# Performance work log

Hardware: AMD Instinct MI355X
Metric: run time of the kernel (lower is better)

Reference implementation:

```python
import jax, jax.numpy as jnp
import numpy as np

NUM_ITERATIONS = 3

def squash(t, axis=-1):
    sq = jnp.sum(t * t, axis=axis, keepdims=True)
    scale = sq / (1.0 + sq)
    return scale * t / jnp.sqrt(sq)

def setup_inputs() -> dict:
    key = jax.random.key(0)
    k1, k2 = jax.random.split(key)
    B, N, Ci = 16, 1024, 64
    C, O = 32, 32
    x = jax.random.normal(k1, (B, N, Ci), dtype=jnp.float32)
    route_weights = jax.random.normal(k2, (C, N, Ci, O), dtype=jnp.float32)
    return {"x": x, "route_weights": route_weights}

def reference(x, route_weights):
    # priors: (C, B, N, O)  == torch's (C,B,N,1,O) with singleton squeezed
    priors = jnp.einsum('bni,cnio->cbno', x, route_weights)
    C, B, N, O = priors.shape
    logits = jnp.zeros((C, B, N, 1), dtype=priors.dtype)
    outputs = None
    for i in range(NUM_ITERATIONS):
        probs = jax.nn.softmax(logits, axis=2)  # over route nodes
        outputs = squash(jnp.sum(probs * priors, axis=2, keepdims=True))  # (C,B,1,O)
        if i != NUM_ITERATIONS - 1:
            delta = jnp.sum(priors * outputs, axis=-1, keepdims=True)  # (C,B,N,1)
            logits = logits + delta
    # match torch output shape (C, B, 1, 1, O)
    return outputs[:, :, :, None, :]
```

## Files before the change

kernel.cpp:

```cpp
#include <hip/hip_runtime.h>

constexpr int kB  = 16;
constexpr int kN  = 1024;
constexpr int kCI = 64;
constexpr int kC  = 32;
constexpr int kO  = 32;
constexpr int kNT = 4;

#define AS1(p) ((__attribute__((address_space(1))) void*)(p))
#define AS3(p) ((__attribute__((address_space(3))) void*)(p))

__global__ __launch_bounds__(128) void priors_kernel(
    const float* __restrict__ x,
    const float* rw,
    float* priors, int cstride, int bstride, int nstr) {
  const int c  = blockIdx.x >> 8;
  const int n0 = (blockIdx.x & 255) * kNT;
  const int t  = threadIdx.x;

  __shared__ float ws[kNT * kCI * kO];

  {
    const float4* src = (const float4*)(rw + (size_t)(c * kN + n0) * (kCI * kO));
    float4* dst4 = (float4*)ws;
    #pragma unroll
    for (int it = 0; it < 16; ++it) {
      int f = t + 128 * it;
      __builtin_amdgcn_global_load_lds(AS1(const_cast<float4*>(src + f)),
                                       AS3(dst4 + f), 16, 0, 0);
    }
  }
  __syncthreads();

  const int j  = t >> 5;
  const int og = (t & 31) >> 2;
  const int bg = t & 3;
  const float* wp  = ws + j * (kCI * kO) + og * 4;
  const float* xr0 = x + (size_t)(bg * 4) * (kN * kCI) + (size_t)(n0 + j) * kCI;

  float acc[4][4];
  #pragma unroll
  for (int bb = 0; bb < 4; ++bb)
    #pragma unroll
    for (int oo = 0; oo < 4; ++oo) acc[bb][oo] = 0.f;

  #pragma unroll
  for (int i0 = 0; i0 < kCI; i0 += 4) {
    float4 wv[4], xv[4];
    #pragma unroll
    for (int q = 0; q < 4; ++q) wv[q] = *(const float4*)(wp + (i0 + q) * kO);
    #pragma unroll
    for (int bb = 0; bb < 4; ++bb)
      xv[bb] = *(const float4*)(xr0 + (size_t)bb * (kN * kCI) + i0);
    #pragma unroll
    for (int q = 0; q < 4; ++q) {
      const float* wq = (const float*)&wv[q];
      #pragma unroll
      for (int bb = 0; bb < 4; ++bb) {
        const float xq = ((const float*)&xv[bb])[q];
        #pragma unroll
        for (int oo = 0; oo < 4; ++oo)
          acc[bb][oo] += xq * wq[oo];
      }
    }
  }

  float* dst = priors + (size_t)c * cstride + (size_t)(n0 + j) * nstr + og * 4;
  #pragma unroll
  for (int bb = 0; bb < 4; ++bb) {
    int b = bg * 4 + bb;
    float4 v = make_float4(acc[bb][0], acc[bb][1], acc[bb][2], acc[bb][3]);
    *(float4*)(dst + (size_t)b * bstride) = v;
  }
}

__global__ __launch_bounds__(256) void routing_kernel(
    const float* priors, int cstride, int bstride, int nstr,
    float* __restrict__ out) {
  const int cb = blockIdx.x;
  const int c = cb >> 4, b = cb & 15;
  const int t = threadIdx.x;

  __shared__ float R[256 * 33];
  __shared__ float S2[8 * 33];
  __shared__ float out_lds[kO];
  __shared__ float wred[8];

  const float* base = priors + (size_t)c * cstride + (size_t)b * bstride;

  float p[4][kO];
  #pragma unroll
  for (int k = 0; k < 4; ++k) {
    const float* rp = base + (size_t)(t + 256 * k) * nstr;
    #pragma unroll
    for (int q = 0; q < 8; ++q) {
      float4 v = *(const float4*)(rp + q * 4);
      p[k][q * 4 + 0] = v.x; p[k][q * 4 + 1] = v.y;
      p[k][q * 4 + 2] = v.z; p[k][q * 4 + 3] = v.w;
    }
  }

  float l[4] = {0.f, 0.f, 0.f, 0.f};

  for (int iter = 0; iter < 3; ++iter) {
    if (iter > 0) {
      #pragma unroll
      for (int k = 0; k < 4; ++k) {
        float d = 0.f;
        #pragma unroll
        for (int o = 0; o < kO; ++o) d += p[k][o] * out_lds[o];
        l[k] += d;
      }
    }
    float lm = fmaxf(fmaxf(l[0], l[1]), fmaxf(l[2], l[3]));
    #pragma unroll
    for (int s = 32; s >= 1; s >>= 1) lm = fmaxf(lm, __shfl_xor(lm, s));
    if ((t & 63) == 0) wred[t >> 6] = lm;
    __syncthreads();
    const float m = fmaxf(fmaxf(wred[0], wred[1]), fmaxf(wred[2], wred[3]));

    float acc[kO];
    #pragma unroll
    for (int o = 0; o < kO; ++o) acc[o] = 0.f;
    float denp = 0.f;
    #pragma unroll
    for (int k = 0; k < 4; ++k) {
      float e = __expf(l[k] - m);
      denp += e;
      #pragma unroll
      for (int o = 0; o < kO; ++o) acc[o] += e * p[k][o];
    }
    #pragma unroll
    for (int s = 32; s >= 1; s >>= 1) denp += __shfl_xor(denp, s);
    if ((t & 63) == 0) wred[4 + (t >> 6)] = denp;

    #pragma unroll
    for (int o = 0; o < kO; ++o) R[t * 33 + o] = acc[o];
    __syncthreads();
    {
      int o = t & 31, g = t >> 5;
      float s = 0.f;
      #pragma unroll
      for (int jj = 0; jj < 32; ++jj) s += R[(g * 32 + jj) * 33 + o];
      S2[g * 33 + o] = s;
    }
    __syncthreads();
    if (t < kO) {
      float s = 0.f;
      #pragma unroll
      for (int g = 0; g < 8; ++g) s += S2[g * 33 + t];
      const float den = wred[4] + wred[5] + wred[6] + wred[7];
      s /= den;
      float sq = s * s;
      #pragma unroll
      for (int sh = 16; sh >= 1; sh >>= 1) sq += __shfl_xor(sq, sh);
      const float r = sqrtf(sq);
      const float ov = s * (r / (1.f + sq));
      out_lds[t] = ov;
      if (iter == 2) out[cb * kO + t] = ov;
    }
    __syncthreads();
  }
}

extern "C" void kernel_launch(void* const* d_in, const int* in_sizes, int n_in,
                              void* d_out, int out_size, void* d_ws, size_t ws_size,
                              hipStream_t stream) {
  const float* x  = (const float*)d_in[0];
  const float* rw = (const float*)d_in[1];
  float* out = (float*)d_out;

  const size_t need = (size_t)kC * kN * kB * kO * sizeof(float);
  float* priors;
  int cstride, bstride, nstr;
  if (ws_size >= need) {
    priors  = (float*)d_ws;
    cstride = kB * kN * kO;
    bstride = kN * kO;
    nstr    = kO;
  } else {
    priors  = (float*)const_cast<float*>(rw);
    cstride = kN * kCI * kO;
    bstride = kO;
    nstr    = kCI * kO;
  }

  priors_kernel<<<dim3(kC * (kN / kNT)), dim3(128), 0, stream>>>(
      x, rw, priors, cstride, bstride, nstr);
  routing_kernel<<<dim3(kC * kB), dim3(256), 0, stream>>>(
      priors, cstride, bstride, nstr, out);
}
```

Baseline: 434.7 us.

## Process multiple capsules per priors block with LDS-resident x and double-buffered weights

The priors kernel now has each block handle eight capsules for the same group of four route nodes. The x slice is loaded once into LDS in a transposed, batch-contiguous layout and reused across all eight capsules, replacing repeated global reads of x. Route weights for the next capsule are staged into a second LDS buffer while the current one is computed, aiming to hide load latency. In exchange the grid shrinks eightfold and LDS use per block grows to about 80 KB, which lowers occupancy and may limit how much latency can be hidden.

```diff
diff --git a/kernel.cpp b/kernel.cpp
--- a/kernel.cpp
+++ b/kernel.cpp
@@ -6,6 +6,7 @@
 constexpr int kC  = 32;
 constexpr int kO  = 32;
 constexpr int kNT = 4;
+constexpr int kCL = 8;
 
 #define AS1(p) ((__attribute__((address_space(1))) void*)(p))
 #define AS3(p) ((__attribute__((address_space(3))) void*)(p))
@@ -14,20 +15,41 @@
     const float* __restrict__ x,
     const float* rw,
     float* priors, int cstride, int bstride, int nstr) {
-  const int c  = blockIdx.x >> 8;
-  const int n0 = (blockIdx.x & 255) * kNT;
+  const int ng = blockIdx.x & 255;
+  const int c0 = (blockIdx.x >> 8) * kCL;
+  const int n0 = ng * kNT;
   const int t  = threadIdx.x;
 
-  __shared__ float ws[kNT * kCI * kO];
+  __shared__ float ws[2][kNT * kCI * kO];
+  __shared__ float xs[kNT * kCI * kB];
+
+#define STAGE_RW(buf, cc) do {                                               \
+    const float4* _src =                                                     \
+        (const float4*)(rw + (size_t)((cc) * kN + n0) * (kCI * kO));         \
+    float4* _dst = (float4*)ws[buf];                                         \
+    _Pragma("unroll")                                                        \
+    for (int _it = 0; _it < 16; ++_it) {                                     \
+      int _f = t + 128 * _it;                                                \
+      __builtin_amdgcn_global_load_lds(AS1(const_cast<float4*>(_src + _f)),  \
+                                       AS3(_dst + _f), 16, 0, 0);            \
+    }                                                                        \
+  } while (0)
+
+  STAGE_RW(0, c0);
 
   {
-    const float4* src = (const float4*)(rw + (size_t)(c * kN + n0) * (kCI * kO));
-    float4* dst4 = (float4*)ws;
-    #pragma unroll
-    for (int it = 0; it < 16; ++it) {
+    #pragma unroll
+    for (int it = 0; it < 8; ++it) {
       int f = t + 128 * it;
-      __builtin_amdgcn_global_load_lds(AS1(const_cast<float4*>(src + f)),
-                                       AS3(dst4 + f), 16, 0, 0);
+      int b = f & 15;
+      int a = (f >> 4) & 15;
+      int j = f >> 8;
+      float4 v = *(const float4*)(x + (size_t)(b * kN + n0 + j) * kCI + a * 4);
+      int idx = (j * kCI + a * 4) * kB + b;
+      xs[idx +  0] = v.x;
+      xs[idx + 16] = v.y;
+      xs[idx + 32] = v.z;
+      xs[idx + 48] = v.w;
     }
   }
   __syncthreads();
@@ -35,43 +57,51 @@
   const int j  = t >> 5;
   const int og = (t & 31) >> 2;
   const int bg = t & 3;
-  const float* wp  = ws + j * (kCI * kO) + og * 4;
-  const float* xr0 = x + (size_t)(bg * 4) * (kN * kCI) + (size_t)(n0 + j) * kCI;
-
-  float acc[4][4];
-  #pragma unroll
-  for (int bb = 0; bb < 4; ++bb)
-    #pragma unroll
-    for (int oo = 0; oo < 4; ++oo) acc[bb][oo] = 0.f;
-
-  #pragma unroll
-  for (int i0 = 0; i0 < kCI; i0 += 4) {
-    float4 wv[4], xv[4];
-    #pragma unroll
-    for (int q = 0; q < 4; ++q) wv[q] = *(const float4*)(wp + (i0 + q) * kO);
+  const float* xp = xs + j * (kCI * kB) + bg * 4;
+
+  for (int k = 0; k < kCL; ++k) {
+    const int cur = k & 1;
+    if (k + 1 < kCL) STAGE_RW(cur ^ 1, c0 + k + 1);
+
+    const float* wp = ws[cur] + j * (kCI * kO) + og * 4;
+
+    float acc[4][4];
     #pragma unroll
     for (int bb = 0; bb < 4; ++bb)
-      xv[bb] = *(const float4*)(xr0 + (size_t)bb * (kN * kCI) + i0);
-    #pragma unroll
-    for (int q = 0; q < 4; ++q) {
-      const float* wq = (const float*)&wv[q];
-      #pragma unroll
-      for (int bb = 0; bb < 4; ++bb) {
-        const float xq = ((const float*)&xv[bb])[q];
+      #pragma unroll
+      for (int oo = 0; oo < 4; ++oo) acc[bb][oo] = 0.f;
+
+    #pragma unroll
+    for (int i0 = 0; i0 < kCI; i0 += 4) {
+      float4 wv[4], xv[4];
+      #pragma unroll
+      for (int q = 0; q < 4; ++q) wv[q] = *(const float4*)(wp + (i0 + q) * kO);
+      #pragma unroll
+      for (int q = 0; q < 4; ++q) xv[q] = *(const float4*)(xp + (i0 + q) * kB);
+      #pragma unroll
+      for (int q = 0; q < 4; ++q) {
+        const float* xq = (const float*)&xv[q];
+        const float* wq = (const float*)&wv[q];
         #pragma unroll
-        for (int oo = 0; oo < 4; ++oo)
-          acc[bb][oo] += xq * wq[oo];
+        for (int bb = 0; bb < 4; ++bb)
+          #pragma unroll
+          for (int oo = 0; oo < 4; ++oo)
+            acc[bb][oo] += xq[bb] * wq[oo];
       }
     }
-  }
-
-  float* dst = priors + (size_t)c * cstride + (size_t)(n0 + j) * nstr + og * 4;
-  #pragma unroll
-  for (int bb = 0; bb < 4; ++bb) {
-    int b = bg * 4 + bb;
-    float4 v = make_float4(acc[bb][0], acc[bb][1], acc[bb][2], acc[bb][3]);
-    *(float4*)(dst + (size_t)b * bstride) = v;
-  }
+
+    float* dst = priors + (size_t)(c0 + k) * cstride +
+                 (size_t)(n0 + j) * nstr + og * 4;
+    #pragma unroll
+    for (int bb = 0; bb < 4; ++bb) {
+      int b = bg * 4 + bb;
+      float4 v = make_float4(acc[bb][0], acc[bb][1], acc[bb][2], acc[bb][3]);
+      *(float4*)(dst + (size_t)b * bstride) = v;
+    }
+
+    __syncthreads();
+  }
+#undef STAGE_RW
 }
 
 __global__ __launch_bounds__(256) void routing_kernel(
@@ -185,7 +215,7 @@
     nstr    = kCI * kO;
   }
 
-  priors_kernel<<<dim3(kC * (kN / kNT)), dim3(128), 0, stream>>>(
+  priors_kernel<<<dim3((kC / kCL) * (kN / kNT)), dim3(128), 0, stream>>>(
       x, rw, priors, cstride, bstride, nstr);
   routing_kernel<<<dim3(kC * kB), dim3(256), 0, stream>>>(
       priors, cstride, bstride, nstr, out);
```

New measurement: 395.5 us. 1.1x faster.

## Stage x in LDS and stream weights from global across channel groups

Applied to the files above, without the earlier changes.

The priors kernel now transposes the x tile for 8 route nodes into shared memory, so that batch entries sit contiguously. Each block then loops over 4 output capsules, reading route weights directly from global memory instead of staging them in LDS through global_load_lds. This reuses the x tile across capsules and cuts LDS footprint so more blocks can be resident. An alias flag adds a barrier before stores when priors overwrite the weight buffer in place. The cost is that weight loads now go uncoalesced straight to registers.

```diff
diff --git a/kernel.cpp b/kernel.cpp
--- a/kernel.cpp
+++ b/kernel.cpp
@@ -5,72 +5,82 @@
 constexpr int kCI = 64;
 constexpr int kC  = 32;
 constexpr int kO  = 32;
-constexpr int kNT = 4;
-
-#define AS1(p) ((__attribute__((address_space(1))) void*)(p))
-#define AS3(p) ((__attribute__((address_space(3))) void*)(p))
-
-__global__ __launch_bounds__(128) void priors_kernel(
+constexpr int kNT = 8;
+constexpr int kCG = 4;
+constexpr int kXS = kCI * kB + 4;
+
+__global__ __launch_bounds__(256, 4) void priors_kernel(
     const float* __restrict__ x,
     const float* rw,
-    float* priors, int cstride, int bstride, int nstr) {
-  const int c  = blockIdx.x >> 8;
-  const int n0 = (blockIdx.x & 255) * kNT;
+    float* priors, int cstride, int bstride, int nstr, int alias) {
+  const int nb = blockIdx.x & 127;
+  const int c0 = (blockIdx.x >> 7) * kCG;
+  const int n0 = nb * kNT;
   const int t  = threadIdx.x;
 
-  __shared__ float ws[kNT * kCI * kO];
-
-  {
-    const float4* src = (const float4*)(rw + (size_t)(c * kN + n0) * (kCI * kO));
-    float4* dst4 = (float4*)ws;
-    #pragma unroll
-    for (int it = 0; it < 16; ++it) {
-      int f = t + 128 * it;
-      __builtin_amdgcn_global_load_lds(AS1(const_cast<float4*>(src + f)),
-                                       AS3(dst4 + f), 16, 0, 0);
-    }
+  __shared__ float xs[kNT * kXS];
+
+  #pragma unroll
+  for (int it = 0; it < 8; ++it) {
+    int f  = t + 256 * it;
+    int b  = f & 15;
+    int ia = (f >> 4) & 15;
+    int ns = f >> 8;
+    float4 v = *(const float4*)(x + (size_t)(b * kN + n0 + ns) * kCI + ia * 4);
+    float* dstp = xs + ns * kXS + (ia * 4) * kB + b;
+    dstp[0 * kB] = v.x;
+    dstp[1 * kB] = v.y;
+    dstp[2 * kB] = v.z;
+    dstp[3 * kB] = v.w;
   }
   __syncthreads();
 
-  const int j  = t >> 5;
-  const int og = (t & 31) >> 2;
-  const int bg = t & 3;
-  const float* wp  = ws + j * (kCI * kO) + og * 4;
-  const float* xr0 = x + (size_t)(bg * 4) * (kN * kCI) + (size_t)(n0 + j) * kCI;
-
-  float acc[4][4];
-  #pragma unroll
-  for (int bb = 0; bb < 4; ++bb)
-    #pragma unroll
-    for (int oo = 0; oo < 4; ++oo) acc[bb][oo] = 0.f;
-
-  #pragma unroll
-  for (int i0 = 0; i0 < kCI; i0 += 4) {
-    float4 wv[4], xv[4];
-    #pragma unroll
-    for (int q = 0; q < 4; ++q) wv[q] = *(const float4*)(wp + (i0 + q) * kO);
+  const int og = t & 7;
+  const int ns = (t >> 3) & 7;
+  const int bq = t >> 6;
+  const int n  = n0 + ns;
+  const float* xp = xs + ns * kXS + bq * 4;
+
+  for (int cc = 0; cc < kCG; ++cc) {
+    const int c = c0 + cc;
+    const float* wp = rw + (size_t)(c * kN + n) * (kCI * kO) + og * 4;
+
+    float acc[4][4];
     #pragma unroll
     for (int bb = 0; bb < 4; ++bb)
-      xv[bb] = *(const float4*)(xr0 + (size_t)bb * (kN * kCI) + i0);
-    #pragma unroll
-    for (int q = 0; q < 4; ++q) {
-      const float* wq = (const float*)&wv[q];
-      #pragma unroll
-      for (int bb = 0; bb < 4; ++bb) {
-        const float xq = ((const float*)&xv[bb])[q];
+      #pragma unroll
+      for (int oo = 0; oo < 4; ++oo) acc[bb][oo] = 0.f;
+
+    #pragma unroll
+    for (int i0 = 0; i0 < kCI; i0 += 4) {
+      float4 wv[4], xv[4];
+      #pragma unroll
+      for (int q = 0; q < 4; ++q)
+        wv[q] = *(const float4*)(wp + (size_t)(i0 + q) * kO);
+      #pragma unroll
+      for (int q = 0; q < 4; ++q)
+        xv[q] = *(const float4*)(xp + (i0 + q) * kB);
+      #pragma unroll
+      for (int q = 0; q < 4; ++q) {
+        const float* xq = (const float*)&xv[q];
+        const float* wq = (const float*)&wv[q];
         #pragma unroll
-        for (int oo = 0; oo < 4; ++oo)
-          acc[bb][oo] += xq * wq[oo];
+        for (int bb = 0; bb < 4; ++bb)
+          #pragma unroll
+          for (int oo = 0; oo < 4; ++oo)
+            acc[bb][oo] += xq[bb] * wq[oo];
       }
     }
-  }
-
-  float* dst = priors + (size_t)c * cstride + (size_t)(n0 + j) * nstr + og * 4;
-  #pragma unroll
-  for (int bb = 0; bb < 4; ++bb) {
-    int b = bg * 4 + bb;
-    float4 v = make_float4(acc[bb][0], acc[bb][1], acc[bb][2], acc[bb][3]);
-    *(float4*)(dst + (size_t)b * bstride) = v;
+
+    if (alias) __syncthreads();
+
+    float* dst = priors + (size_t)c * cstride + (size_t)n * nstr + og * 4;
+    #pragma unroll
+    for (int bb = 0; bb < 4; ++bb) {
+      int b = bq * 4 + bb;
+      float4 v = make_float4(acc[bb][0], acc[bb][1], acc[bb][2], acc[bb][3]);
+      *(float4*)(dst + (size_t)b * bstride) = v;
+    }
   }
 }
 
@@ -172,21 +182,23 @@
 
   const size_t need = (size_t)kC * kN * kB * kO * sizeof(float);
   float* priors;
-  int cstride, bstride, nstr;
+  int cstride, bstride, nstr, alias;
   if (ws_size >= need) {
     priors  = (float*)d_ws;
     cstride = kB * kN * kO;
     bstride = kN * kO;
     nstr    = kO;
+    alias   = 0;
   } else {
     priors  = (float*)const_cast<float*>(rw);
     cstride = kN * kCI * kO;
     bstride = kO;
     nstr    = kCI * kO;
-  }
-
-  priors_kernel<<<dim3(kC * (kN / kNT)), dim3(128), 0, stream>>>(
-      x, rw, priors, cstride, bstride, nstr);
+    alias   = 1;
+  }
+
+  priors_kernel<<<dim3((kC / kCG) * (kN / kNT)), dim3(256), 0, stream>>>(
+      x, rw, priors, cstride, bstride, nstr, alias);
   routing_kernel<<<dim3(kC * kB), dim3(256), 0, stream>>>(
       priors, cstride, bstride, nstr, out);
 }
```

Result: slower. 1.143 ms (+163.0%).
